# Kernel tuning notes

Measured on AMD Instinct MI355X. Metric: run time of the kernel, lower is better.

Reference implementation:

```python
import jax, jax.numpy as jnp
import numpy as np

N_EMBED = 1024
N_HEADS = 16
HEAD_SIZE = N_EMBED // N_HEADS
BLOCK_SIZE = 256
LN_EPS = 1e-5


def _layernorm(x, g, b):
    mu = jnp.mean(x, axis=-1, keepdims=True)
    var = jnp.var(x, axis=-1, keepdims=True)
    return (x - mu) * jax.lax.rsqrt(var + LN_EPS) * g + b


def setup_inputs() -> dict:
    key = jax.random.key(0)
    ks = jax.random.split(key, 12)
    B, T, C, H, D = 64, 256, N_EMBED, N_HEADS, HEAD_SIZE
    s = lambda fan_in: 1.0 / np.sqrt(fan_in)
    return {
        "x": jax.random.normal(ks[0], (B, T, C), jnp.float32),
        # per-head Q/K/V projections (bias=False in torch), stacked over heads
        "Wq": jax.random.uniform(ks[1], (H, C, D), jnp.float32, -s(C), s(C)),
        "Wk": jax.random.uniform(ks[2], (H, C, D), jnp.float32, -s(C), s(C)),
        "Wv": jax.random.uniform(ks[3], (H, C, D), jnp.float32, -s(C), s(C)),
        "Wproj": jax.random.uniform(ks[4], (C, C), jnp.float32, -s(C), s(C)),
        "bproj": jax.random.uniform(ks[5], (C,), jnp.float32, -s(C), s(C)),
        "W1": jax.random.uniform(ks[6], (C, 4 * C), jnp.float32, -s(C), s(C)),
        "b1": jax.random.uniform(ks[7], (4 * C,), jnp.float32, -s(C), s(C)),
        "W2": jax.random.uniform(ks[8], (4 * C, C), jnp.float32, -s(4 * C), s(4 * C)),
        "b2": jax.random.uniform(ks[9], (C,), jnp.float32, -s(4 * C), s(4 * C)),
        "ln1_g": jnp.ones((C,), jnp.float32),
        "ln1_b": jnp.zeros((C,), jnp.float32),
        "ln2_g": jnp.ones((C,), jnp.float32),
        "ln2_b": jnp.zeros((C,), jnp.float32),
    }


def reference(x, Wq, Wk, Wv, Wproj, bproj, W1, b1, W2, b2, ln1_g, ln1_b, ln2_g, ln2_b):
    B, T, C = x.shape
    # --- self-attention sub-block ---
    h = _layernorm(x, ln1_g, ln1_b)
    q = jnp.einsum("btc,hcd->bhtd", h, Wq)
    k = jnp.einsum("btc,hcd->bhtd", h, Wk)
    v = jnp.einsum("btc,hcd->bhtd", h, Wv)
    # NOTE: original scales by C**-0.5 with C = n_embed (full dim), not head_size
    scores = jnp.einsum("bhtd,bhsd->bhts", q, k) * (C ** -0.5)
    causal = jnp.tril(jnp.ones((T, T), bool))
    scores = jnp.where(causal, scores, -jnp.inf)
    wei = jax.nn.softmax(scores, axis=-1)
    attn = jnp.einsum("bhts,bhsd->bhtd", wei, v)  # [B,H,T,D]
    attn = attn.transpose(0, 2, 1, 3).reshape(B, T, C)  # concat heads
    x = x + attn @ Wproj + bproj
    # --- feed-forward sub-block ---
    h2 = _layernorm(x, ln2_g, ln2_b)
    ffn = jax.nn.relu(h2 @ W1 + b1) @ W2 + b2
    return x + ffn
```

## Files before the change

### kernel.cpp

```cpp
#include <hip/hip_runtime.h>
#include <stdint.h>

using u16 = unsigned short;
using u32 = unsigned int;

typedef __attribute__((ext_vector_type(8))) short s16x8;
typedef __attribute__((ext_vector_type(4))) float f32x4;

__device__ __forceinline__ float bf2f(u16 u) { u32 t = (u32)u << 16; float f; __builtin_memcpy(&f, &t, 4); return f; }
__device__ __forceinline__ u16 f2bf(float f) {
  u32 u; __builtin_memcpy(&u, &f, 4);
  return (u16)((u + 0x7fffu + ((u >> 16) & 1u)) >> 16);
}

__device__ __forceinline__ void gload_lds16(const void* g, void* l) {
  __builtin_amdgcn_global_load_lds((const __attribute__((address_space(1))) void*)g,
                                   (__attribute__((address_space(3))) void*)l, 16, 0, 0);
}

__global__ __launch_bounds__(256)
void transpose_pack(const float* __restrict__ in, u16* __restrict__ out,
                    int R, int Cc, long in_bs, long out_bs)
{
  __shared__ float tile[32][33];
  in  += (size_t)blockIdx.z * in_bs;
  out += (size_t)blockIdx.z * out_bs;
  const int r0 = blockIdx.x * 32, c0 = blockIdx.y * 32;
  const int tx = threadIdx.x & 31, ty = threadIdx.x >> 5;
#pragma unroll
  for (int i = 0; i < 4; ++i) {
    int r = ty + i * 8;
    tile[r][tx] = in[(size_t)(r0 + r) * Cc + c0 + tx];
  }
  __syncthreads();
#pragma unroll
  for (int i = 0; i < 4; ++i) {
    int c = ty + i * 8;
    out[(size_t)(c0 + c) * R + r0 + tx] = f2bf(tile[tx][c]);
  }
}

template <int IN>
__global__ __launch_bounds__(256)
void ln_to_bf16(const void* __restrict__ xv, const float* __restrict__ g,
                const float* __restrict__ bta, u16* __restrict__ out)
{
  const int row = blockIdx.x, tid = threadIdx.x;
  float4 v;
  if constexpr (IN == 0) {
    v = ((const float4*)((const float*)xv + (size_t)row * 1024))[tid];
  } else {
    uint2 u = ((const uint2*)((const u16*)xv + (size_t)row * 1024))[tid];
    v.x = bf2f((u16)(u.x & 0xffff)); v.y = bf2f((u16)(u.x >> 16));
    v.z = bf2f((u16)(u.y & 0xffff)); v.w = bf2f((u16)(u.y >> 16));
  }
  float s  = v.x + v.y + v.z + v.w;
  float ss = v.x * v.x + v.y * v.y + v.z * v.z + v.w * v.w;
#pragma unroll
  for (int m = 1; m < 64; m <<= 1) {
    s  += __shfl_xor(s, m);
    ss += __shfl_xor(ss, m);
  }
  __shared__ float red[8];
  const int wave = tid >> 6, lane = tid & 63;
  if (lane == 0) { red[wave] = s; red[4 + wave] = ss; }
  __syncthreads();
  s  = red[0] + red[1] + red[2] + red[3];
  ss = red[4] + red[5] + red[6] + red[7];
  const float mu  = s * (1.f / 1024.f);
  const float var = ss * (1.f / 1024.f) - mu * mu;
  const float rs  = rsqrtf(var + 1e-5f);
  const float4 gg = ((const float4*)g)[tid];
  const float4 bb = ((const float4*)bta)[tid];
  u32 w0 = (u32)f2bf((v.x - mu) * rs * gg.x + bb.x) | ((u32)f2bf((v.y - mu) * rs * gg.y + bb.y) << 16);
  u32 w1 = (u32)f2bf((v.z - mu) * rs * gg.z + bb.z) | ((u32)f2bf((v.w - mu) * rs * gg.w + bb.w) << 16);
  u32* outp = (u32*)(out + (size_t)row * 1024 + tid * 4);
  outp[0] = w0; outp[1] = w1;
}

template <int EPI>
__global__ __launch_bounds__(512, 2)
void gemm8p(const u16* __restrict__ A, const u16* __restrict__ B, void* __restrict__ Cv,
            const float* __restrict__ bias, const void* __restrict__ resid,
            int M, int N, int K, int CM, int CN, int XN)
{
  __shared__ u16 lds[65536];
  const int NT = K >> 6;
  const int tid = threadIdx.x;
  const int lane = tid & 63, wv = tid >> 6;
  const int wr = wv >> 2, wc = wv & 3;
  const int r = lane & 15, kg = lane >> 4;

  const int bid = blockIdx.x;
  const int x = bid & 7, i = bid >> 3;
  const int bm = (x / XN) * CM + i / CN;
  const int bn = (x % XN) * CN + i % CN;

  const u16* Ab = A + (size_t)bm * 256 * K;
  const u16* Bb = B + (size_t)bn * 256 * K;

  const u32 ldsb = (u32)(uintptr_t)lds;
  const u32 segb = (u32)((kg ^ (r >> 1)) << 4);
  const u32 abase = ldsb + (u32)((wr * 128 + r) * 128) + segb;
  const u32 bbase = ldsb + 65536u + (u32)((wc * 64 + r) * 128) + segb;

  f32x4 acc[8][4];
#pragma unroll
  for (int m = 0; m < 8; ++m)
#pragma unroll
    for (int n = 0; n < 4; ++n) acc[m][n] = f32x4{0.f, 0.f, 0.f, 0.f};

  auto stage = [&](const u16* src, int u, int h, int base_u16) {
#pragma unroll
    for (int jj = 0; jj < 2; ++jj) {
      int ci = jj * 512 + tid;
      int rl = ci >> 3;
      int sseg = (ci & 7) ^ ((rl >> 1) & 7);
      gload_lds16(src + (size_t)(h * 128 + rl) * K + u * 64 + sseg * 8,
                  &lds[base_u16 + h * 8192 + ci * 8]);
    }
  };

#define DSR(d, a, o) asm volatile("ds_read_b128 %0, %1 offset:" o : "=v"(d) : "v"(a))
#define ISSUE12(aR, bR) \
  DSR(bv0, bR, "0"); DSR(bv1, bR, "2048"); DSR(bv2, bR, "4096"); DSR(bv3, bR, "6144"); \
  DSR(av0, aR, "0"); DSR(av1, aR, "2048"); DSR(av2, aR, "4096"); DSR(av3, aR, "6144"); \
  DSR(av4, aR, "8192"); DSR(av5, aR, "10240"); DSR(av6, aR, "12288"); DSR(av7, aR, "14336")
#define MM(m, n) acc[m][n] = __builtin_amdgcn_mfma_f32_16x16x32_bf16(av##m, bv##n, acc[m][n], 0, 0, 0)
#define RUNG(m, cnt) \
  asm volatile("s_waitcnt lgkmcnt(" #cnt ")" ::: "memory"); \
  __builtin_amdgcn_sched_barrier(0); \
  MM(m, 0); MM(m, 1); MM(m, 2); MM(m, 3)
#define LADDER() \
  RUNG(0, 7); RUNG(1, 6); RUNG(2, 5); RUNG(3, 4); \
  RUNG(4, 3); RUNG(5, 2); RUNG(6, 1); RUNG(7, 0)

  stage(Ab, 0, 0, 0);      stage(Ab, 0, 1, 0);
  stage(Bb, 0, 0, 32768);  stage(Bb, 0, 1, 32768);
  asm volatile("s_waitcnt vmcnt(0)" ::: "memory");
  __builtin_amdgcn_s_barrier();

  for (int t = 0; t < NT; ++t) {
    const int buf = t & 1;
    const bool s1 = (t + 1) < NT;
    const int nb = (buf ^ 1) * 16384;
    const u32 aA0 = abase + (u32)(buf * 32768);
    const u32 aB0 = bbase + (u32)(buf * 32768);
    const u32 aA1 = aA0 ^ 64u;
    const u32 aB1 = aB0 ^ 64u;

    if (s1) {
      stage(Ab, t + 1, 0, nb);           stage(Ab, t + 1, 1, nb);
      stage(Bb, t + 1, 0, 32768 + nb);   stage(Bb, t + 1, 1, 32768 + nb);
    }
    __builtin_amdgcn_sched_barrier(0);
    __builtin_amdgcn_s_setprio(1);
    {
      s16x8 av0, av1, av2, av3, av4, av5, av6, av7, bv0, bv1, bv2, bv3;
      ISSUE12(aA0, aB0);
      LADDER();
    }
    {
      s16x8 av0, av1, av2, av3, av4, av5, av6, av7, bv0, bv1, bv2, bv3;
      ISSUE12(aA1, aB1);
      LADDER();
    }
    __builtin_amdgcn_s_setprio(0);
    __builtin_amdgcn_sched_barrier(0);
    asm volatile("s_waitcnt vmcnt(0)" ::: "memory");
    __builtin_amdgcn_s_barrier();
  }

#pragma unroll
  for (int m = 0; m < 8; ++m) {
#pragma unroll
    for (int n = 0; n < 4; ++n) {
#pragma unroll
      for (int j = 0; j < 4; ++j) {
        int row = bm * 256 + wr * 128 + m * 16 + kg * 4 + j;
        int col = bn * 256 + wc * 64 + n * 16 + r;
        size_t idx = (size_t)row * N + col;
        float v = acc[m][n][j];
        if constexpr (EPI == 0) {
          ((u16*)Cv)[idx] = f2bf(v);
        } else if constexpr (EPI == 1) {
          ((u16*)Cv)[idx] = f2bf(v + bias[col] + ((const float*)resid)[idx]);
        } else if constexpr (EPI == 2) {
          ((u16*)Cv)[idx] = f2bf(fmaxf(v + bias[col], 0.f));
        } else {
          ((float*)Cv)[idx] = v + bias[col] + bf2f(((const u16*)resid)[idx]);
        }
      }
    }
  }
#undef DSR
#undef ISSUE12
#undef MM
#undef RUNG
#undef LADDER
}

__global__ __launch_bounds__(256)
void attn_mfma(const u16* __restrict__ qkv, u16* __restrict__ outc)
{
  const int bh = blockIdx.x, b = bh >> 4, h = bh & 15;
  const int tid = threadIdx.x;
  const int lane = tid & 63, w = tid >> 6;
  const int r = lane & 15, kg = lane >> 4;

  __shared__ u16 Ks[64 * 64];
  __shared__ u16 Vt[64 * 72];
  __shared__ u16 P[4][64 * 72];

  const u16* qbase = qkv + (size_t)(b * 256) * 3072 + h * 64;

  s16x8 qf[4][2];
#pragma unroll
  for (int m = 0; m < 4; ++m)
#pragma unroll
    for (int ks = 0; ks < 2; ++ks)
      qf[m][ks] = *(const s16x8*)(qbase + (size_t)(w * 64 + m * 16 + r) * 3072 + ks * 32 + kg * 8);

  f32x4 of[4][4];
  float mrun[4][4], lrun[4][4];
#pragma unroll
  for (int m = 0; m < 4; ++m) {
#pragma unroll
    for (int n = 0; n < 4; ++n) of[m][n] = f32x4{0.f, 0.f, 0.f, 0.f};
#pragma unroll
    for (int j = 0; j < 4; ++j) { mrun[m][j] = -1e30f; lrun[m][j] = 0.f; }
  }

  const float cexp = 0.03125f * 1.4426950408889634f;

  for (int kt = 0; kt < 4; ++kt) {
#pragma unroll
    for (int jj = 0; jj < 2; ++jj) {
      int ci = jj * 256 + tid;
      int key = ci >> 3, seg = ci & 7;
      int sseg = seg ^ (key & 7);
      gload_lds16(qkv + (size_t)(b * 256 + kt * 64 + key) * 3072 + 1024 + h * 64 + sseg * 8,
                  &Ks[ci * 8]);
    }
    {
      int row = tid >> 2, q = tid & 3;
      const u16* vg = qkv + (size_t)(b * 256 + kt * 64 + row) * 3072 + 2048 + h * 64 + q * 16;
      union { uint4 u[2]; u16 s[16]; } vv;
      vv.u[0] = *(const uint4*)vg;
      vv.u[1] = *(const uint4*)(vg + 8);
#pragma unroll
      for (int i = 0; i < 16; ++i)
        Vt[(q * 16 + i) * 72 + row] = vv.s[i];
    }
    __syncthreads();

    if (w >= kt) {
      f32x4 s[4][4];
#pragma unroll
      for (int m = 0; m < 4; ++m)
#pragma unroll
        for (int n = 0; n < 4; ++n) s[m][n] = f32x4{0.f, 0.f, 0.f, 0.f};
#pragma unroll
      for (int ks = 0; ks < 2; ++ks) {
        s16x8 kb[4];
#pragma unroll
        for (int n = 0; n < 4; ++n) {
          int row = n * 16 + r;
          int sseg = (ks * 4 + kg) ^ (row & 7);
          kb[n] = *(const s16x8*)&Ks[row * 64 + sseg * 8];
        }
#pragma unroll
        for (int m = 0; m < 4; ++m)
#pragma unroll
          for (int n = 0; n < 4; ++n)
            s[m][n] = __builtin_amdgcn_mfma_f32_16x16x32_bf16(qf[m][ks], kb[n], s[m][n], 0, 0, 0);
      }
      if (kt == w) {
#pragma unroll
        for (int m = 0; m < 4; ++m)
#pragma unroll
          for (int n = 0; n < 4; ++n)
#pragma unroll
            for (int j = 0; j < 4; ++j)
              if (n * 16 + r > m * 16 + kg * 4 + j) s[m][n][j] = -1e30f;
      }
#pragma unroll
      for (int m = 0; m < 4; ++m) {
        float rm[4], rsc[4], ls[4];
#pragma unroll
        for (int j = 0; j < 4; ++j) {
          rm[j] = fmaxf(fmaxf(s[m][0][j], s[m][1][j]), fmaxf(s[m][2][j], s[m][3][j]));
          rm[j] = fmaxf(rm[j], __shfl_xor(rm[j], 1));
          rm[j] = fmaxf(rm[j], __shfl_xor(rm[j], 2));
          rm[j] = fmaxf(rm[j], __shfl_xor(rm[j], 4));
          rm[j] = fmaxf(rm[j], __shfl_xor(rm[j], 8));
          float mnew = fmaxf(mrun[m][j], rm[j]);
          rsc[j] = exp2f((mrun[m][j] - mnew) * cexp);
          mrun[m][j] = mnew;
          ls[j] = 0.f;
        }
#pragma unroll
        for (int n = 0; n < 4; ++n)
#pragma unroll
          for (int j = 0; j < 4; ++j) {
            float p = exp2f((s[m][n][j] - mrun[m][j]) * cexp);
            ls[j] += p;
            P[w][(m * 16 + kg * 4 + j) * 72 + n * 16 + r] = f2bf(p);
          }
#pragma unroll
        for (int j = 0; j < 4; ++j) {
          ls[j] += __shfl_xor(ls[j], 1);
          ls[j] += __shfl_xor(ls[j], 2);
          ls[j] += __shfl_xor(ls[j], 4);
          ls[j] += __shfl_xor(ls[j], 8);
          lrun[m][j] = lrun[m][j] * rsc[j] + ls[j];
        }
#pragma unroll
        for (int n = 0; n < 4; ++n)
#pragma unroll
          for (int j = 0; j < 4; ++j)
            of[m][n][j] *= rsc[j];
      }
#pragma unroll
      for (int kk = 0; kk < 2; ++kk) {
        s16x8 pa[4], vb[4];
#pragma unroll
        for (int m = 0; m < 4; ++m)
          pa[m] = *(const s16x8*)&P[w][(m * 16 + r) * 72 + kk * 32 + kg * 8];
#pragma unroll
        for (int n = 0; n < 4; ++n)
          vb[n] = *(const s16x8*)&Vt[(n * 16 + r) * 72 + kk * 32 + kg * 8];
#pragma unroll
        for (int m = 0; m < 4; ++m)
#pragma unroll
          for (int n = 0; n < 4; ++n)
            of[m][n] = __builtin_amdgcn_mfma_f32_16x16x32_bf16(pa[m], vb[n], of[m][n], 0, 0, 0);
      }
    }
    __syncthreads();
  }

#pragma unroll
  for (int m = 0; m < 4; ++m) {
    float inv[4];
#pragma unroll
    for (int j = 0; j < 4; ++j) inv[j] = 1.f / lrun[m][j];
#pragma unroll
    for (int n = 0; n < 4; ++n)
#pragma unroll
      for (int j = 0; j < 4; ++j) {
        int row = b * 256 + w * 64 + m * 16 + kg * 4 + j;
        outc[(size_t)row * 1024 + h * 64 + n * 16 + r] = f2bf(of[m][n][j] * inv[j]);
      }
  }
}

extern "C" void kernel_launch(void* const* d_in, const int* in_sizes, int n_in,
                              void* d_out, int out_size, void* d_ws, size_t ws_size,
                              hipStream_t stream) {
  (void)in_sizes; (void)n_in; (void)out_size; (void)ws_size;
  const float* x     = (const float*)d_in[0];
  const float* Wq    = (const float*)d_in[1];
  const float* Wk    = (const float*)d_in[2];
  const float* Wv    = (const float*)d_in[3];
  const float* Wproj = (const float*)d_in[4];
  const float* bproj = (const float*)d_in[5];
  const float* W1    = (const float*)d_in[6];
  const float* b1    = (const float*)d_in[7];
  const float* W2    = (const float*)d_in[8];
  const float* b2    = (const float*)d_in[9];
  const float* ln1g  = (const float*)d_in[10];
  const float* ln1b  = (const float*)d_in[11];
  const float* ln2g  = (const float*)d_in[12];
  const float* ln2b  = (const float*)d_in[13];
  float* out = (float*)d_out;

  char* ws = (char*)d_ws;
  u16*   WqkvT  = (u16*)(ws + 0);
  u16*   WprojT = (u16*)(ws + 6291456);
  u16*   W1T    = (u16*)(ws + 8388608);
  u16*   W2T    = (u16*)(ws + 16777216);
  u16*   hb     = (u16*)(ws + 25165824);
  u16*   qkvb   = (u16*)(ws + 58720256);
  u16*   x2     = (u16*)(ws + 159383552);
  u16*   h2     = (u16*)(ws + 226492416);
  u16*   ffn1   = (u16*)(ws + 25165824);
  u16*   attnout = hb;

  const int M = 16384;

  transpose_pack<<<dim3(32, 2, 16), 256, 0, stream>>>(Wq, WqkvT,           1024, 64, 65536, 65536);
  transpose_pack<<<dim3(32, 2, 16), 256, 0, stream>>>(Wk, WqkvT + 1048576, 1024, 64, 65536, 65536);
  transpose_pack<<<dim3(32, 2, 16), 256, 0, stream>>>(Wv, WqkvT + 2097152, 1024, 64, 65536, 65536);
  transpose_pack<<<dim3(32, 32, 1), 256, 0, stream>>>(Wproj, WprojT, 1024, 1024, 0, 0);
  transpose_pack<<<dim3(32, 128, 1), 256, 0, stream>>>(W1, W1T, 1024, 4096, 0, 0);
  transpose_pack<<<dim3(128, 32, 1), 256, 0, stream>>>(W2, W2T, 4096, 1024, 0, 0);

  ln_to_bf16<0><<<M, 256, 0, stream>>>(x, ln1g, ln1b, hb);

  gemm8p<0><<<768, 512, 0, stream>>>(hb, WqkvT, qkvb, nullptr, nullptr, M, 3072, 1024, 16, 6, 2);

  attn_mfma<<<1024, 256, 0, stream>>>(qkvb, attnout);

  gemm8p<1><<<256, 512, 0, stream>>>(attnout, WprojT, x2, bproj, x, M, 1024, 1024, 8, 4, 1);

  ln_to_bf16<1><<<M, 256, 0, stream>>>(x2, ln2g, ln2b, h2);

  gemm8p<2><<<1024, 512, 0, stream>>>(h2, W1T, ffn1, b1, nullptr, M, 4096, 1024, 16, 8, 2);

  gemm8p<3><<<256, 512, 0, stream>>>(ffn1, W2T, out, b2, x2, M, 1024, 4096, 8, 4, 1);
}
```

Baseline: 557.1 us.

## Add single-buffered GEMM variant with mid-tile prefetch for FFN GEMMs

Introduces gemm1b, which uses one LDS buffer (64KB instead of 128KB) so that two 512-thread blocks can fit per CU. The next K-tile is loaded after all LDS reads of the current tile finish, overlapping with the remaining half of the MFMAs. Both FFN GEMMs switch to this kernel, and the epilogue is factored into a shared helper. In exchange, there is less load/compute overlap per block and an extra barrier per K step.

```diff
diff --git a/kernel.cpp b/kernel.cpp
--- a/kernel.cpp
+++ b/kernel.cpp
@@ -78,49 +78,6 @@
   outp[0] = w0; outp[1] = w1;
 }
 
-template <int EPI>
-__global__ __launch_bounds__(512, 2)
-void gemm8p(const u16* __restrict__ A, const u16* __restrict__ B, void* __restrict__ Cv,
-            const float* __restrict__ bias, const void* __restrict__ resid,
-            int M, int N, int K, int CM, int CN, int XN)
-{
-  __shared__ u16 lds[65536];
-  const int NT = K >> 6;
-  const int tid = threadIdx.x;
-  const int lane = tid & 63, wv = tid >> 6;
-  const int wr = wv >> 2, wc = wv & 3;
-  const int r = lane & 15, kg = lane >> 4;
-
-  const int bid = blockIdx.x;
-  const int x = bid & 7, i = bid >> 3;
-  const int bm = (x / XN) * CM + i / CN;
-  const int bn = (x % XN) * CN + i % CN;
-
-  const u16* Ab = A + (size_t)bm * 256 * K;
-  const u16* Bb = B + (size_t)bn * 256 * K;
-
-  const u32 ldsb = (u32)(uintptr_t)lds;
-  const u32 segb = (u32)((kg ^ (r >> 1)) << 4);
-  const u32 abase = ldsb + (u32)((wr * 128 + r) * 128) + segb;
-  const u32 bbase = ldsb + 65536u + (u32)((wc * 64 + r) * 128) + segb;
-
-  f32x4 acc[8][4];
-#pragma unroll
-  for (int m = 0; m < 8; ++m)
-#pragma unroll
-    for (int n = 0; n < 4; ++n) acc[m][n] = f32x4{0.f, 0.f, 0.f, 0.f};
-
-  auto stage = [&](const u16* src, int u, int h, int base_u16) {
-#pragma unroll
-    for (int jj = 0; jj < 2; ++jj) {
-      int ci = jj * 512 + tid;
-      int rl = ci >> 3;
-      int sseg = (ci & 7) ^ ((rl >> 1) & 7);
-      gload_lds16(src + (size_t)(h * 128 + rl) * K + u * 64 + sseg * 8,
-                  &lds[base_u16 + h * 8192 + ci * 8]);
-    }
-  };
-
 #define DSR(d, a, o) asm volatile("ds_read_b128 %0, %1 offset:" o : "=v"(d) : "v"(a))
 #define ISSUE12(aR, bR) \
   DSR(bv0, bR, "0"); DSR(bv1, bR, "2048"); DSR(bv2, bR, "4096"); DSR(bv3, bR, "6144"); \
@@ -135,42 +92,11 @@
   RUNG(0, 7); RUNG(1, 6); RUNG(2, 5); RUNG(3, 4); \
   RUNG(4, 3); RUNG(5, 2); RUNG(6, 1); RUNG(7, 0)
 
-  stage(Ab, 0, 0, 0);      stage(Ab, 0, 1, 0);
-  stage(Bb, 0, 0, 32768);  stage(Bb, 0, 1, 32768);
-  asm volatile("s_waitcnt vmcnt(0)" ::: "memory");
-  __builtin_amdgcn_s_barrier();
-
-  for (int t = 0; t < NT; ++t) {
-    const int buf = t & 1;
-    const bool s1 = (t + 1) < NT;
-    const int nb = (buf ^ 1) * 16384;
-    const u32 aA0 = abase + (u32)(buf * 32768);
-    const u32 aB0 = bbase + (u32)(buf * 32768);
-    const u32 aA1 = aA0 ^ 64u;
-    const u32 aB1 = aB0 ^ 64u;
-
-    if (s1) {
-      stage(Ab, t + 1, 0, nb);           stage(Ab, t + 1, 1, nb);
-      stage(Bb, t + 1, 0, 32768 + nb);   stage(Bb, t + 1, 1, 32768 + nb);
-    }
-    __builtin_amdgcn_sched_barrier(0);
-    __builtin_amdgcn_s_setprio(1);
-    {
-      s16x8 av0, av1, av2, av3, av4, av5, av6, av7, bv0, bv1, bv2, bv3;
-      ISSUE12(aA0, aB0);
-      LADDER();
-    }
-    {
-      s16x8 av0, av1, av2, av3, av4, av5, av6, av7, bv0, bv1, bv2, bv3;
-      ISSUE12(aA1, aB1);
-      LADDER();
-    }
-    __builtin_amdgcn_s_setprio(0);
-    __builtin_amdgcn_sched_barrier(0);
-    asm volatile("s_waitcnt vmcnt(0)" ::: "memory");
-    __builtin_amdgcn_s_barrier();
-  }
-
+template <int EPI>
+__device__ __forceinline__ void gemm_epilogue(f32x4 (&acc)[8][4], void* Cv, const float* bias,
+                                              const void* resid, int N, int bm, int bn,
+                                              int wr, int wc, int r, int kg)
+{
 #pragma unroll
   for (int m = 0; m < 8; ++m) {
 #pragma unroll
@@ -193,12 +119,176 @@
       }
     }
   }
+}
+
+template <int EPI>
+__global__ __launch_bounds__(512, 2)
+void gemm8p(const u16* __restrict__ A, const u16* __restrict__ B, void* __restrict__ Cv,
+            const float* __restrict__ bias, const void* __restrict__ resid,
+            int M, int N, int K, int CM, int CN, int XN)
+{
+  __shared__ u16 lds[65536];
+  const int NT = K >> 6;
+  const int tid = threadIdx.x;
+  const int lane = tid & 63, wv = tid >> 6;
+  const int wr = wv >> 2, wc = wv & 3;
+  const int r = lane & 15, kg = lane >> 4;
+
+  const int bid = blockIdx.x;
+  const int x = bid & 7, i = bid >> 3;
+  const int bm = (x / XN) * CM + i / CN;
+  const int bn = (x % XN) * CN + i % CN;
+
+  const u16* Ab = A + (size_t)bm * 256 * K;
+  const u16* Bb = B + (size_t)bn * 256 * K;
+
+  const u32 ldsb = (u32)(uintptr_t)lds;
+  const u32 segb = (u32)((kg ^ (r >> 1)) << 4);
+  const u32 abase = ldsb + (u32)((wr * 128 + r) * 128) + segb;
+  const u32 bbase = ldsb + 65536u + (u32)((wc * 64 + r) * 128) + segb;
+
+  f32x4 acc[8][4];
+#pragma unroll
+  for (int m = 0; m < 8; ++m)
+#pragma unroll
+    for (int n = 0; n < 4; ++n) acc[m][n] = f32x4{0.f, 0.f, 0.f, 0.f};
+
+  auto stage = [&](const u16* src, int u, int h, int base_u16) {
+#pragma unroll
+    for (int jj = 0; jj < 2; ++jj) {
+      int ci = jj * 512 + tid;
+      int rl = ci >> 3;
+      int sseg = (ci & 7) ^ ((rl >> 1) & 7);
+      gload_lds16(src + (size_t)(h * 128 + rl) * K + u * 64 + sseg * 8,
+                  &lds[base_u16 + h * 8192 + ci * 8]);
+    }
+  };
+
+  stage(Ab, 0, 0, 0);      stage(Ab, 0, 1, 0);
+  stage(Bb, 0, 0, 32768);  stage(Bb, 0, 1, 32768);
+  asm volatile("s_waitcnt vmcnt(0)" ::: "memory");
+  __builtin_amdgcn_s_barrier();
+
+  for (int t = 0; t < NT; ++t) {
+    const int buf = t & 1;
+    const bool s1 = (t + 1) < NT;
+    const int nb = (buf ^ 1) * 16384;
+    const u32 aA0 = abase + (u32)(buf * 32768);
+    const u32 aB0 = bbase + (u32)(buf * 32768);
+
+    if (s1) {
+      stage(Ab, t + 1, 0, nb);           stage(Ab, t + 1, 1, nb);
+      stage(Bb, t + 1, 0, 32768 + nb);   stage(Bb, t + 1, 1, 32768 + nb);
+    }
+    __builtin_amdgcn_sched_barrier(0);
+    __builtin_amdgcn_s_setprio(1);
+    {
+      s16x8 av0, av1, av2, av3, av4, av5, av6, av7, bv0, bv1, bv2, bv3;
+      ISSUE12(aA0, aB0);
+      LADDER();
+    }
+    {
+      s16x8 av0, av1, av2, av3, av4, av5, av6, av7, bv0, bv1, bv2, bv3;
+      ISSUE12(aA0 ^ 64u, aB0 ^ 64u);
+      LADDER();
+    }
+    __builtin_amdgcn_s_setprio(0);
+    __builtin_amdgcn_sched_barrier(0);
+    asm volatile("s_waitcnt vmcnt(0)" ::: "memory");
+    __builtin_amdgcn_s_barrier();
+  }
+  gemm_epilogue<EPI>(acc, Cv, bias, resid, N, bm, bn, wr, wc, r, kg);
+}
+
+template <int EPI>
+__global__ __launch_bounds__(512, 2)
+void gemm1b(const u16* __restrict__ A, const u16* __restrict__ B, void* __restrict__ Cv,
+            const float* __restrict__ bias, const void* __restrict__ resid,
+            int M, int N, int K, int CM, int CN, int XN)
+{
+  __shared__ u16 lds[32768];
+  const int NT = K >> 6;
+  const int tid = threadIdx.x;
+  const int lane = tid & 63, wv = tid >> 6;
+  const int wr = wv >> 2, wc = wv & 3;
+  const int r = lane & 15, kg = lane >> 4;
+
+  const int bid = blockIdx.x;
+  const int x = bid & 7, i = bid >> 3;
+  const int bm = (x / XN) * CM + i / CN;
+  const int bn = (x % XN) * CN + i % CN;
+
+  const u16* Ab = A + (size_t)bm * 256 * K;
+  const u16* Bb = B + (size_t)bn * 256 * K;
+
+  const u32 ldsb = (u32)(uintptr_t)lds;
+  const u32 segb = (u32)((kg ^ (r >> 1)) << 4);
+  const u32 aA0 = ldsb + (u32)((wr * 128 + r) * 128) + segb;
+  const u32 aB0 = ldsb + 32768u + (u32)((wc * 64 + r) * 128) + segb;
+
+  f32x4 acc[8][4];
+#pragma unroll
+  for (int m = 0; m < 8; ++m)
+#pragma unroll
+    for (int n = 0; n < 4; ++n) acc[m][n] = f32x4{0.f, 0.f, 0.f, 0.f};
+
+  auto stage = [&](const u16* src, int u, int h, int base_u16) {
+#pragma unroll
+    for (int jj = 0; jj < 2; ++jj) {
+      int ci = jj * 512 + tid;
+      int rl = ci >> 3;
+      int sseg = (ci & 7) ^ ((rl >> 1) & 7);
+      gload_lds16(src + (size_t)(h * 128 + rl) * K + u * 64 + sseg * 8,
+                  &lds[base_u16 + h * 8192 + ci * 8]);
+    }
+  };
+
+  stage(Ab, 0, 0, 0);      stage(Ab, 0, 1, 0);
+  stage(Bb, 0, 0, 16384);  stage(Bb, 0, 1, 16384);
+  asm volatile("s_waitcnt vmcnt(0)" ::: "memory");
+  __builtin_amdgcn_s_barrier();
+
+  for (int t = 0; t < NT; ++t) {
+    const bool s1 = (t + 1) < NT;
+    __builtin_amdgcn_s_setprio(1);
+    {
+      s16x8 av0, av1, av2, av3, av4, av5, av6, av7, bv0, bv1, bv2, bv3;
+      ISSUE12(aA0, aB0);
+      LADDER();
+    }
+    {
+      s16x8 av0, av1, av2, av3, av4, av5, av6, av7, bv0, bv1, bv2, bv3;
+      ISSUE12(aA0 ^ 64u, aB0 ^ 64u);
+      RUNG(0, 7); RUNG(1, 6); RUNG(2, 5); RUNG(3, 4);
+      asm volatile("s_waitcnt lgkmcnt(0)" ::: "memory");
+      __builtin_amdgcn_sched_barrier(0);
+      __builtin_amdgcn_s_setprio(0);
+      __builtin_amdgcn_s_barrier();
+      __builtin_amdgcn_sched_barrier(0);
+      if (s1) {
+        stage(Ab, t + 1, 0, 0);      stage(Ab, t + 1, 1, 0);
+        stage(Bb, t + 1, 0, 16384);  stage(Bb, t + 1, 1, 16384);
+      }
+      __builtin_amdgcn_sched_barrier(0);
+      __builtin_amdgcn_s_setprio(1);
+      MM(4, 0); MM(4, 1); MM(4, 2); MM(4, 3);
+      MM(5, 0); MM(5, 1); MM(5, 2); MM(5, 3);
+      MM(6, 0); MM(6, 1); MM(6, 2); MM(6, 3);
+      MM(7, 0); MM(7, 1); MM(7, 2); MM(7, 3);
+    }
+    __builtin_amdgcn_s_setprio(0);
+    __builtin_amdgcn_sched_barrier(0);
+    asm volatile("s_waitcnt vmcnt(0)" ::: "memory");
+    __builtin_amdgcn_s_barrier();
+  }
+  gemm_epilogue<EPI>(acc, Cv, bias, resid, N, bm, bn, wr, wc, r, kg);
+}
+
 #undef DSR
 #undef ISSUE12
 #undef MM
 #undef RUNG
 #undef LADDER
-}
 
 __global__ __launch_bounds__(256)
 void attn_mfma(const u16* __restrict__ qkv, u16* __restrict__ outc)
@@ -406,7 +496,7 @@
 
   ln_to_bf16<1><<<M, 256, 0, stream>>>(x2, ln2g, ln2b, h2);
 
-  gemm8p<2><<<1024, 512, 0, stream>>>(h2, W1T, ffn1, b1, nullptr, M, 4096, 1024, 16, 8, 2);
-
-  gemm8p<3><<<256, 512, 0, stream>>>(ffn1, W2T, out, b2, x2, M, 1024, 4096, 8, 4, 1);
-}
+  gemm1b<2><<<1024, 512, 0, stream>>>(h2, W1T, ffn1, b1, nullptr, M, 4096, 1024, 16, 8, 2);
+
+  gemm1b<3><<<256, 512, 0, stream>>>(ffn1, W2T, out, b2, x2, M, 1024, 4096, 8, 4, 1);
+}
```

Result: slower. 611.4 us (+9.8%).
